# Kernel optimization log

Hardware: AMD Instinct MI355X
Metric: run time of the kernel (lower is better)

The kernel has to match this reference:

```python
import jax, jax.numpy as jnp
import numpy as np

B, L, HID = 128, 256, 768
HID2 = 2 * HID
CDIM, SDIM, NPROJ = 192, 128, 128
FDIM = CDIM + SDIM + 1
BIG = 1e9  # finite pad so sorted invalid tokens go last without inf/nan issues


def setup_inputs() -> dict:
    key = jax.random.key(0)
    ks = jax.random.split(key, 12)
    H = jax.random.normal(ks[0], (B, L, HID), dtype=jnp.float32)
    tt = jax.random.randint(ks[1], (B, L), 0, 2, dtype=jnp.int32)
    m = jnp.ones((B, L), dtype=jnp.int32)
    s = 1.0 / np.sqrt(HID2)
    Wc = jax.random.uniform(ks[2], (CDIM, HID2), minval=-s, maxval=s, dtype=jnp.float32)
    bc = jax.random.uniform(ks[3], (CDIM,), minval=-s, maxval=s, dtype=jnp.float32)
    Ws = jax.random.uniform(ks[4], (SDIM, HID2), minval=-s, maxval=s, dtype=jnp.float32)
    bs = jax.random.uniform(ks[5], (SDIM,), minval=-s, maxval=s, dtype=jnp.float32)
    gate = jnp.array([0.5], dtype=jnp.float32)
    ln_g = jnp.ones((FDIM,), dtype=jnp.float32)
    ln_b = jnp.zeros((FDIM,), dtype=jnp.float32)
    sc = 1.0 / np.sqrt(FDIM)
    Wcls = jax.random.uniform(ks[6], (2, FDIM), minval=-sc, maxval=sc, dtype=jnp.float32)
    bcls = jax.random.uniform(ks[7], (2,), minval=-sc, maxval=sc, dtype=jnp.float32)
    d = jax.random.normal(ks[8], (NPROJ, HID), dtype=jnp.float32)
    proj_dirs = d / jnp.linalg.norm(d, axis=1, keepdims=True)
    return {"H": H, "tt": tt, "m": m, "Wc": Wc, "bc": bc, "Ws": Ws, "bs": bs,
            "gate": gate, "ln_g": ln_g, "ln_b": ln_b, "Wcls": Wcls, "bcls": bcls,
            "proj_dirs": proj_dirs}


def _forward(H, tt, m, Wc, bc, Ws, bs, gate, ln_g, ln_b, Wcls, bcls, proj_dirs):
    mask0 = (tt == 0) & (m == 1)  # [B,L]
    mask1 = (tt == 1) & (m == 1)
    f0 = mask0.astype(H.dtype)
    f1 = mask1.astype(H.dtype)
    cls = H[:, 0]  # [B,HID]
    mean0 = jnp.einsum('blh,bl->bh', H, f0) / jnp.clip(f0.sum(1, keepdims=True), 1.0)
    mean1 = jnp.einsum('blh,bl->bh', H, f1) / jnp.clip(f1.sum(1, keepdims=True), 1.0)
    rep = jnp.concatenate([cls, mean0 - mean1], axis=1)  # [B,2*HID]
    C = rep @ Wc.T + bc
    S = rep @ Ws.T + bs
    g = jax.nn.sigmoid(gate)  # [1]
    fused = jnp.concatenate([C * (1.0 - g), S * g], axis=1)

    # max-sliced W1 between token-type-0 and token-type-1 token sets, batched.
    P = jnp.einsum('blh,ph->blp', H, proj_dirs)  # [B,L,NPROJ]
    x0 = jnp.sort(jnp.where(mask0[..., None], P, BIG), axis=1)  # valid tokens first
    x1 = jnp.sort(jnp.where(mask1[..., None], P, BIG), axis=1)
    n0 = mask0.sum(1)
    n1 = mask1.sum(1)
    mcnt = jnp.minimum(n0, n1)  # [B]
    rmask = (jnp.arange(L)[None, :] < mcnt[:, None])[..., None]  # [B,L,1]
    diff = jnp.where(rmask, x0, 0.0) - jnp.where(rmask, x1, 0.0)
    mean_abs = jnp.abs(diff).sum(1) / jnp.maximum(mcnt, 1)[:, None].astype(P.dtype)  # [B,NPROJ]
    d_ot = mean_abs.max(axis=1, keepdims=True)  # [B,1]

    feat = jnp.concatenate([fused, d_ot], axis=1)  # [B,FDIM]
    mu = feat.mean(-1, keepdims=True)
    var = feat.var(-1, keepdims=True)
    normed = (feat - mu) * jax.lax.rsqrt(var + 1e-5) * ln_g + ln_b
    return normed @ Wcls.T + bcls  # [B,2]


def reference(H, tt, m, Wc, bc, Ws, bs, gate, ln_g, ln_b, Wcls, bcls, proj_dirs):
    return _forward(H, tt, m, Wc, bc, Ws, bs, gate, ln_g, ln_b, Wcls, bcls, proj_dirs)
```

## Files before the change

kernel.cpp:

```cpp
#include <hip/hip_runtime.h>
#include <cmath>

#define B_   128
#define L_   256
#define HID_ 768
#define HID2_ 1536
#define CDIM_ 192
#define SDIM_ 128
#define NPROJ_ 128
#define FDIM_ 321

typedef __attribute__((ext_vector_type(8))) short bf16x8;
typedef __attribute__((ext_vector_type(4))) float f32x4;

__device__ inline unsigned short bf_hi_trunc(float x) {
    return (unsigned short)(__float_as_uint(x) >> 16);
}
__device__ inline float bf2f(unsigned short s) {
    return __uint_as_float(((unsigned int)s) << 16);
}
__device__ inline unsigned short f2bf_rne(float x) {
    unsigned int u = __float_as_uint(x);
    unsigned int r = (u + 0x7fff + ((u >> 16) & 1)) >> 16;
    return (unsigned short)r;
}

__global__ __launch_bounds__(192) void stats_part(
    const float* __restrict__ H, const int* __restrict__ tt,
    const int* __restrict__ mm, float* __restrict__ part)
{
    int b  = blockIdx.x >> 3;
    int pr = blockIdx.x & 7;
    int tid = threadIdx.x;

    __shared__ float sf0[32], sf1[32];
    if (tid < 32) {
        int l = pr * 32 + tid;
        int t = tt[b * L_ + l];
        int mv = mm[b * L_ + l];
        sf0[tid] = (t == 0 && mv == 1) ? 1.f : 0.f;
        sf1[tid] = (t == 1 && mv == 1) ? 1.f : 0.f;
    }
    __syncthreads();

    const float* Hb = H + ((size_t)(b * L_ + pr * 32)) * HID_;
    float4 a0 = make_float4(0.f, 0.f, 0.f, 0.f);
    float4 a1 = make_float4(0.f, 0.f, 0.f, 0.f);
    for (int l = 0; l < 32; ++l) {
        float4 x = *(const float4*)(Hb + (size_t)l * HID_ + tid * 4);
        float f0 = sf0[l], f1 = sf1[l];
        a0.x += x.x * f0; a0.y += x.y * f0; a0.z += x.z * f0; a0.w += x.w * f0;
        a1.x += x.x * f1; a1.y += x.y * f1; a1.z += x.z * f1; a1.w += x.w * f1;
    }
    float* dst = part + ((size_t)(b * 8 + pr)) * HID2_;
    *(float4*)(dst + tid * 4) = a0;
    *(float4*)(dst + HID_ + tid * 4) = a1;
}

__global__ __launch_bounds__(256) void stats_fin(
    const float* __restrict__ H, const int* __restrict__ tt,
    const int* __restrict__ mm, const float* __restrict__ part,
    float* __restrict__ rep)
{
    int b = blockIdx.x;
    int tid = threadIdx.x;
    int t = tt[b * L_ + tid];
    int mv = mm[b * L_ + tid];
    int n0 = __syncthreads_count(t == 0 && mv == 1);
    int n1 = __syncthreads_count(t == 1 && mv == 1);
    float r0 = 1.f / fmaxf((float)n0, 1.f);
    float r1 = 1.f / fmaxf((float)n1, 1.f);

    const float* pp = part + (size_t)b * 8 * HID2_;
    for (int h = tid; h < HID_; h += 256) {
        float a0 = 0.f, a1 = 0.f;
#pragma unroll
        for (int q = 0; q < 8; ++q) {
            a0 += pp[(size_t)q * HID2_ + h];
            a1 += pp[(size_t)q * HID2_ + HID_ + h];
        }
        rep[(size_t)b * HID2_ + h] = H[(size_t)b * L_ * HID_ + h];
        rep[(size_t)b * HID2_ + HID_ + h] = a0 * r0 - a1 * r1;
    }
}

__global__ __launch_bounds__(256) void head_kernel(
    const float* __restrict__ rep, const float* __restrict__ Wc,
    const float* __restrict__ bc, const float* __restrict__ Ws,
    const float* __restrict__ bs, const float* __restrict__ gate,
    float* __restrict__ fused)
{
    int w = blockIdx.x * 4 + (threadIdx.x >> 6);
    int lane = threadIdx.x & 63;
    int b = w / (CDIM_ + SDIM_);
    int o = w % (CDIM_ + SDIM_);
    bool isC = (o < CDIM_);
    const float4* wr = (const float4*)(isC ? (Wc + (size_t)o * HID2_)
                                           : (Ws + (size_t)(o - CDIM_) * HID2_));
    const float4* rp = (const float4*)(rep + (size_t)b * HID2_);
    float acc = 0.f;
#pragma unroll
    for (int u = 0; u < 6; ++u) {
        int k4 = lane + u * 64;
        float4 a = rp[k4];
        float4 ww = wr[k4];
        acc += a.x * ww.x + a.y * ww.y + a.z * ww.z + a.w * ww.w;
    }
    for (int off = 32; off; off >>= 1) acc += __shfl_xor(acc, off, 64);
    if (lane == 0) {
        float g = 1.0f / (1.0f + expf(-gate[0]));
        float bias = isC ? bc[o] : bs[o - CDIM_];
        float scale = isC ? (1.0f - g) : g;
        fused[(size_t)b * (CDIM_ + SDIM_) + o] = (acc + bias) * scale;
    }
}

__global__ __launch_bounds__(256) void conv_proj(
    const float* __restrict__ Pd, unsigned short* __restrict__ hi,
    unsigned short* __restrict__ lo)
{
    int i = blockIdx.x * 256 + threadIdx.x;
    float4 v = ((const float4*)Pd)[i];
    ushort4 h, l;
    h.x = bf_hi_trunc(v.x); l.x = f2bf_rne(v.x - bf2f(h.x));
    h.y = bf_hi_trunc(v.y); l.y = f2bf_rne(v.y - bf2f(h.y));
    h.z = bf_hi_trunc(v.z); l.z = f2bf_rne(v.z - bf2f(h.z));
    h.w = bf_hi_trunc(v.w); l.w = f2bf_rne(v.w - bf2f(h.w));
    ((ushort4*)hi)[i] = h;
    ((ushort4*)lo)[i] = l;
}

#define LDSROW 72
__global__ __launch_bounds__(256, 2) void gemm_mfma(
    const float* __restrict__ H, const unsigned short* __restrict__ Pjh,
    const unsigned short* __restrict__ Pjl, float* __restrict__ Pt)
{
    __shared__ unsigned short Hs[2][64 * LDSROW];

    int tid = threadIdx.x;
    int w = tid >> 6;
    int lane = tid & 63;
    int c = lane & 15;
    int q = lane >> 4;

    int b = blockIdx.x >> 2;
    int lbase = (blockIdx.x & 3) * 64;

    const float* Hbase = H + ((size_t)(b * L_ + lbase)) * HID_;

    int hrow0 = tid >> 3;
    int hc4   = tid & 7;

    const unsigned short* pjh0 = Pjh + (size_t)(w * 32 + c) * HID_ + q * 8;
    const unsigned short* pjh1 = Pjh + (size_t)(w * 32 + 16 + c) * HID_ + q * 8;
    const unsigned short* pjl0 = Pjl + (size_t)(w * 32 + c) * HID_ + q * 8;
    const unsigned short* pjl1 = Pjl + (size_t)(w * 32 + 16 + c) * HID_ + q * 8;

    f32x4 acc[2][4] = {};

    float4 hreg[2];
    uint4 cah[2], cal[2];
    uint4 nah[2], nal[2];

    hreg[0] = *(const float4*)(Hbase + (size_t)hrow0 * HID_ + hc4 * 4);
    hreg[1] = *(const float4*)(Hbase + (size_t)(hrow0 + 32) * HID_ + hc4 * 4);
    cah[0] = *(const uint4*)(pjh0);
    cah[1] = *(const uint4*)(pjh1);
    cal[0] = *(const uint4*)(pjl0);
    cal[1] = *(const uint4*)(pjl1);
#pragma unroll
    for (int u = 0; u < 2; ++u) {
        int row = hrow0 + u * 32;
        float4 v = hreg[u];
        ushort4 h, l;
        h.x = bf_hi_trunc(v.x); l.x = f2bf_rne(v.x - bf2f(h.x));
        h.y = bf_hi_trunc(v.y); l.y = f2bf_rne(v.y - bf2f(h.y));
        h.z = bf_hi_trunc(v.z); l.z = f2bf_rne(v.z - bf2f(h.z));
        h.w = bf_hi_trunc(v.w); l.w = f2bf_rne(v.w - bf2f(h.w));
        *(ushort4*)&Hs[0][row * LDSROW + hc4 * 4]      = h;
        *(ushort4*)&Hs[0][row * LDSROW + 32 + hc4 * 4] = l;
    }
    __syncthreads();

    for (int it = 0; it < 24; ++it) {
        int cur = it & 1;
        int nxt = cur ^ 1;

        if (it + 1 < 24) {
            int k0 = (it + 1) * 32;
            hreg[0] = *(const float4*)(Hbase + (size_t)hrow0 * HID_ + k0 + hc4 * 4);
            hreg[1] = *(const float4*)(Hbase + (size_t)(hrow0 + 32) * HID_ + k0 + hc4 * 4);
            nah[0] = *(const uint4*)(pjh0 + k0);
            nah[1] = *(const uint4*)(pjh1 + k0);
            nal[0] = *(const uint4*)(pjl0 + k0);
            nal[1] = *(const uint4*)(pjl1 + k0);
        }

        bf16x8 bh[4], bl[4];
#pragma unroll
        for (int lt = 0; lt < 4; ++lt) {
            int l = lt * 16 + c;
            bh[lt] = *(const bf16x8*)&Hs[cur][l * LDSROW + q * 8];
            bl[lt] = *(const bf16x8*)&Hs[cur][l * LDSROW + 32 + q * 8];
        }
        bf16x8 ah[2], al[2];
        ah[0] = *(bf16x8*)&cah[0]; ah[1] = *(bf16x8*)&cah[1];
        al[0] = *(bf16x8*)&cal[0]; al[1] = *(bf16x8*)&cal[1];

#pragma unroll
        for (int pt = 0; pt < 2; ++pt)
#pragma unroll
        for (int lt = 0; lt < 4; ++lt) {
            acc[pt][lt] = __builtin_amdgcn_mfma_f32_16x16x32_bf16(ah[pt], bh[lt], acc[pt][lt], 0, 0, 0);
            acc[pt][lt] = __builtin_amdgcn_mfma_f32_16x16x32_bf16(ah[pt], bl[lt], acc[pt][lt], 0, 0, 0);
            acc[pt][lt] = __builtin_amdgcn_mfma_f32_16x16x32_bf16(al[pt], bh[lt], acc[pt][lt], 0, 0, 0);
        }

        if (it + 1 < 24) {
#pragma unroll
            for (int u = 0; u < 2; ++u) {
                int row = hrow0 + u * 32;
                float4 v = hreg[u];
                ushort4 h, l;
                h.x = bf_hi_trunc(v.x); l.x = f2bf_rne(v.x - bf2f(h.x));
                h.y = bf_hi_trunc(v.y); l.y = f2bf_rne(v.y - bf2f(h.y));
                h.z = bf_hi_trunc(v.z); l.z = f2bf_rne(v.z - bf2f(h.z));
                h.w = bf_hi_trunc(v.w); l.w = f2bf_rne(v.w - bf2f(h.w));
                *(ushort4*)&Hs[nxt][row * LDSROW + hc4 * 4]      = h;
                *(ushort4*)&Hs[nxt][row * LDSROW + 32 + hc4 * 4] = l;
            }
            cah[0] = nah[0]; cah[1] = nah[1];
            cal[0] = nal[0]; cal[1] = nal[1];
        }
        __syncthreads();
    }

#pragma unroll
    for (int pt = 0; pt < 2; ++pt)
#pragma unroll
    for (int lt = 0; lt < 4; ++lt)
#pragma unroll
    for (int r = 0; r < 4; ++r) {
        int p = w * 32 + pt * 16 + q * 4 + r;
        int l = lbase + lt * 16 + c;
        Pt[((size_t)(b * NPROJ_ + p)) * L_ + l] = acc[pt][lt][r];
    }
}

__global__ __launch_bounds__(256) void ot_kernel(
    const float* __restrict__ Pt, const int* __restrict__ tt,
    const int* __restrict__ mm, float* __restrict__ dist)
{
    int w = blockIdx.x * 4 + (threadIdx.x >> 6);
    int lane = threadIdx.x & 63;
    int b = w >> 7;
    int p = w & (NPROJ_ - 1);

    float4 pv = *(const float4*)(Pt + ((size_t)(b * NPROJ_ + p)) * L_ + lane * 4);
    int4 t4 = *(const int4*)(tt + (size_t)b * L_ + lane * 4);
    int4 m4 = *(const int4*)(mm + (size_t)b * L_ + lane * 4);

    float pvals[4] = {pv.x, pv.y, pv.z, pv.w};
    int tv[4] = {t4.x, t4.y, t4.z, t4.w};
    int mv[4] = {m4.x, m4.y, m4.z, m4.w};

    unsigned key[4];
#pragma unroll
    for (int r = 0; r < 4; ++r) {
        unsigned u = __float_as_uint(pvals[r]);
        unsigned s = (u & 0x80000000u) ? ~u : (u | 0x80000000u);
        unsigned label = (mv[r] == 1) ? (unsigned)tv[r] : 2u;
        key[r] = (s & ~3u) | label;
    }

    {
        unsigned mn0 = min(key[0], key[1]), mx0 = max(key[0], key[1]);
        key[0] = mn0; key[1] = mx0;
        unsigned mn1 = min(key[2], key[3]), mx1 = max(key[2], key[3]);
        key[2] = mx1; key[3] = mn1;
    }
#pragma unroll
    for (int k = 4; k <= 256; k <<= 1) {
        bool up = (lane & (k >> 2)) == 0;
#pragma unroll
        for (int j = k >> 1; j >= 4; j >>= 1) {
            int lj = j >> 2;
#pragma unroll
            for (int r = 0; r < 4; ++r) {
                unsigned o = (unsigned)__shfl_xor((int)key[r], lj, 64);
                bool lower = (lane & lj) == 0;
                unsigned mn = min(key[r], o), mx = max(key[r], o);
                key[r] = (lower == up) ? mn : mx;
            }
        }
        {
            unsigned mn0 = min(key[0], key[2]), mx0 = max(key[0], key[2]);
            key[0] = up ? mn0 : mx0; key[2] = up ? mx0 : mn0;
            unsigned mn1 = min(key[1], key[3]), mx1 = max(key[1], key[3]);
            key[1] = up ? mn1 : mx1; key[3] = up ? mx1 : mn1;
        }
        {
            unsigned mn0 = min(key[0], key[1]), mx0 = max(key[0], key[1]);
            key[0] = up ? mn0 : mx0; key[1] = up ? mx0 : mn0;
            unsigned mn1 = min(key[2], key[3]), mx1 = max(key[2], key[3]);
            key[2] = up ? mn1 : mx1; key[3] = up ? mx1 : mn1;
        }
    }

    int lab[4];
    float tval[4];
    unsigned sincl[4];
    unsigned run = 0;
#pragma unroll
    for (int r = 0; r < 4; ++r) {
        lab[r] = (int)(key[r] & 3u);
        unsigned s = key[r] & ~3u;
        unsigned u = (s & 0x80000000u) ? (s ^ 0x80000000u) : ~s;
        tval[r] = __uint_as_float(u);
        unsigned unit = ((lab[r] == 0) ? 0x10000u : 0u) | ((lab[r] == 1) ? 1u : 0u);
        run += unit;
        sincl[r] = run;
    }
    unsigned inc = run;
#pragma unroll
    for (int d = 1; d < 64; d <<= 1) {
        unsigned t = (unsigned)__shfl_up((int)inc, d, 64);
        if (lane >= d) inc += t;
    }
    unsigned ex = inc - run;
    unsigned total = (unsigned)__shfl((int)inc, 63, 64);
    int n0 = (int)(total >> 16), n1 = (int)(total & 0xffffu);
    int m = (n0 < n1) ? n0 : n1;

    float ssum = 0.f;
#pragma unroll
    for (int r = 0; r < 4; ++r) {
        unsigned C = ex + sincl[r];
        int c0 = (int)(C >> 16), c1 = (int)(C & 0xffffu);
        int s0 = (lab[r] == 0), s1 = (lab[r] == 1);
        int wi = abs(min(c0, m) - min(c1, m));
        int wp = abs(min(c0 - s0, m) - min(c1 - s1, m));
        ssum += tval[r] * (float)(wp - wi);
    }
    for (int off = 32; off; off >>= 1) ssum += __shfl_xor(ssum, off, 64);
    if (lane == 0) dist[b * NPROJ_ + p] = ssum / (float)((m > 1) ? m : 1);
}

__global__ __launch_bounds__(64) void final_kernel(
    const float* __restrict__ fused, const float* __restrict__ dist,
    const float* __restrict__ ln_g, const float* __restrict__ ln_b,
    const float* __restrict__ Wcls, const float* __restrict__ bcls,
    float* __restrict__ out)
{
    int b = blockIdx.x;
    int lane = threadIdx.x;

    float mx = fmaxf(dist[b * NPROJ_ + lane], dist[b * NPROJ_ + 64 + lane]);
    for (int off = 32; off; off >>= 1) mx = fmaxf(mx, __shfl_xor(mx, off, 64));

    float fv[6];
    float sum = 0.f, sq = 0.f;
#pragma unroll
    for (int u = 0; u < 6; ++u) {
        int j = lane + u * 64;
        float x = 0.f;
        if (j < CDIM_ + SDIM_) x = fused[(size_t)b * (CDIM_ + SDIM_) + j];
        else if (j == CDIM_ + SDIM_) x = mx;
        fv[u] = x;
        if (j < FDIM_) { sum += x; sq += x * x; }
    }
    for (int off = 32; off; off >>= 1) {
        sum += __shfl_xor(sum, off, 64);
        sq  += __shfl_xor(sq,  off, 64);
    }
    float mu = sum / (float)FDIM_;
    float var = sq / (float)FDIM_ - mu * mu;
    float inv = rsqrtf(var + 1e-5f);

    float d0 = 0.f, d1 = 0.f;
#pragma unroll
    for (int u = 0; u < 6; ++u) {
        int j = lane + u * 64;
        if (j < FDIM_) {
            float nx = (fv[u] - mu) * inv * ln_g[j] + ln_b[j];
            d0 += nx * Wcls[j];
            d1 += nx * Wcls[FDIM_ + j];
        }
    }
    for (int off = 32; off; off >>= 1) {
        d0 += __shfl_xor(d0, off, 64);
        d1 += __shfl_xor(d1, off, 64);
    }
    if (lane == 0) {
        out[b * 2 + 0] = d0 + bcls[0];
        out[b * 2 + 1] = d1 + bcls[1];
    }
}

extern "C" void kernel_launch(void* const* d_in, const int* in_sizes, int n_in,
                              void* d_out, int out_size, void* d_ws, size_t ws_size,
                              hipStream_t stream)
{
    const float* H    = (const float*)d_in[0];
    const int*   tt   = (const int*)d_in[1];
    const int*   mm   = (const int*)d_in[2];
    const float* Wc   = (const float*)d_in[3];
    const float* bc   = (const float*)d_in[4];
    const float* Ws   = (const float*)d_in[5];
    const float* bs   = (const float*)d_in[6];
    const float* gate = (const float*)d_in[7];
    const float* ln_g = (const float*)d_in[8];
    const float* ln_b = (const float*)d_in[9];
    const float* Wcls = (const float*)d_in[10];
    const float* bcls = (const float*)d_in[11];
    const float* Pd   = (const float*)d_in[12];
    float* out = (float*)d_out;

    float* ws = (float*)d_ws;
    float* Pt    = ws;
    float* part  = Pt;
    float* rep   = Pt + (size_t)B_ * NPROJ_ * L_;
    float* fused = rep + (size_t)B_ * HID2_;
    float* dist  = fused + (size_t)B_ * (CDIM_ + SDIM_);
    unsigned short* Pjh = (unsigned short*)(dist + (size_t)B_ * NPROJ_);
    unsigned short* Pjl = Pjh + (size_t)NPROJ_ * HID_;

    conv_proj<<<NPROJ_ * HID_ / 4 / 256, 256, 0, stream>>>(Pd, Pjh, Pjl);
    stats_part<<<B_ * 8, 192, 0, stream>>>(H, tt, mm, part);
    stats_fin<<<B_, 256, 0, stream>>>(H, tt, mm, part, rep);
    head_kernel<<<B_ * (CDIM_ + SDIM_) / 4, 256, 0, stream>>>(rep, Wc, bc, Ws, bs, gate, fused);
    gemm_mfma<<<B_ * 4, 256, 0, stream>>>(H, Pjh, Pjl, Pt);
    ot_kernel<<<B_ * NPROJ_ / 4, 256, 0, stream>>>(Pt, tt, mm, dist);
    final_kernel<<<B_, 64, 0, stream>>>(fused, dist, ln_g, ln_b, Wcls, bcls, out);
}
```

Before: 248.6 us.

## Fuse projection conversion with stats, and stats finalize with classifier head

Merges the bf16 split of projection directions into the partial-stats kernel as extra blocks. It also merges the stats finalization and the C/S head matvec into one per-batch kernel that keeps the representation in shared memory. This removes two launches and the global rep buffer, and gives the partial sums their own workspace so they are no longer aliased with Pt. The cost is that the head now runs on only 128 blocks, each looping over 320 weight rows, which reduces parallelism.

```diff
diff --git a/kernel.cpp b/kernel.cpp
--- a/kernel.cpp
+++ b/kernel.cpp
@@ -25,13 +25,28 @@
     return (unsigned short)r;
 }
 
-__global__ __launch_bounds__(192) void stats_part(
+__global__ __launch_bounds__(192) void pre_kernel(
+    const float* __restrict__ Pd, unsigned short* __restrict__ Pjh,
+    unsigned short* __restrict__ Pjl,
     const float* __restrict__ H, const int* __restrict__ tt,
     const int* __restrict__ mm, float* __restrict__ part)
 {
-    int b  = blockIdx.x >> 3;
-    int pr = blockIdx.x & 7;
     int tid = threadIdx.x;
+    if (blockIdx.x < 128) {
+        int i = blockIdx.x * 192 + tid;
+        float4 v = ((const float4*)Pd)[i];
+        ushort4 h, l;
+        h.x = bf_hi_trunc(v.x); l.x = f2bf_rne(v.x - bf2f(h.x));
+        h.y = bf_hi_trunc(v.y); l.y = f2bf_rne(v.y - bf2f(h.y));
+        h.z = bf_hi_trunc(v.z); l.z = f2bf_rne(v.z - bf2f(h.z));
+        h.w = bf_hi_trunc(v.w); l.w = f2bf_rne(v.w - bf2f(h.w));
+        ((ushort4*)Pjh)[i] = h;
+        ((ushort4*)Pjl)[i] = l;
+        return;
+    }
+    int bid = blockIdx.x - 128;
+    int b  = bid >> 3;
+    int pr = bid & 7;
 
     __shared__ float sf0[32], sf1[32];
     if (tid < 32) {
@@ -55,79 +70,6 @@
     float* dst = part + ((size_t)(b * 8 + pr)) * HID2_;
     *(float4*)(dst + tid * 4) = a0;
     *(float4*)(dst + HID_ + tid * 4) = a1;
-}
-
-__global__ __launch_bounds__(256) void stats_fin(
-    const float* __restrict__ H, const int* __restrict__ tt,
-    const int* __restrict__ mm, const float* __restrict__ part,
-    float* __restrict__ rep)
-{
-    int b = blockIdx.x;
-    int tid = threadIdx.x;
-    int t = tt[b * L_ + tid];
-    int mv = mm[b * L_ + tid];
-    int n0 = __syncthreads_count(t == 0 && mv == 1);
-    int n1 = __syncthreads_count(t == 1 && mv == 1);
-    float r0 = 1.f / fmaxf((float)n0, 1.f);
-    float r1 = 1.f / fmaxf((float)n1, 1.f);
-
-    const float* pp = part + (size_t)b * 8 * HID2_;
-    for (int h = tid; h < HID_; h += 256) {
-        float a0 = 0.f, a1 = 0.f;
-#pragma unroll
-        for (int q = 0; q < 8; ++q) {
-            a0 += pp[(size_t)q * HID2_ + h];
-            a1 += pp[(size_t)q * HID2_ + HID_ + h];
-        }
-        rep[(size_t)b * HID2_ + h] = H[(size_t)b * L_ * HID_ + h];
-        rep[(size_t)b * HID2_ + HID_ + h] = a0 * r0 - a1 * r1;
-    }
-}
-
-__global__ __launch_bounds__(256) void head_kernel(
-    const float* __restrict__ rep, const float* __restrict__ Wc,
-    const float* __restrict__ bc, const float* __restrict__ Ws,
-    const float* __restrict__ bs, const float* __restrict__ gate,
-    float* __restrict__ fused)
-{
-    int w = blockIdx.x * 4 + (threadIdx.x >> 6);
-    int lane = threadIdx.x & 63;
-    int b = w / (CDIM_ + SDIM_);
-    int o = w % (CDIM_ + SDIM_);
-    bool isC = (o < CDIM_);
-    const float4* wr = (const float4*)(isC ? (Wc + (size_t)o * HID2_)
-                                           : (Ws + (size_t)(o - CDIM_) * HID2_));
-    const float4* rp = (const float4*)(rep + (size_t)b * HID2_);
-    float acc = 0.f;
-#pragma unroll
-    for (int u = 0; u < 6; ++u) {
-        int k4 = lane + u * 64;
-        float4 a = rp[k4];
-        float4 ww = wr[k4];
-        acc += a.x * ww.x + a.y * ww.y + a.z * ww.z + a.w * ww.w;
-    }
-    for (int off = 32; off; off >>= 1) acc += __shfl_xor(acc, off, 64);
-    if (lane == 0) {
-        float g = 1.0f / (1.0f + expf(-gate[0]));
-        float bias = isC ? bc[o] : bs[o - CDIM_];
-        float scale = isC ? (1.0f - g) : g;
-        fused[(size_t)b * (CDIM_ + SDIM_) + o] = (acc + bias) * scale;
-    }
-}
-
-__global__ __launch_bounds__(256) void conv_proj(
-    const float* __restrict__ Pd, unsigned short* __restrict__ hi,
-    unsigned short* __restrict__ lo)
-{
-    int i = blockIdx.x * 256 + threadIdx.x;
-    float4 v = ((const float4*)Pd)[i];
-    ushort4 h, l;
-    h.x = bf_hi_trunc(v.x); l.x = f2bf_rne(v.x - bf2f(h.x));
-    h.y = bf_hi_trunc(v.y); l.y = f2bf_rne(v.y - bf2f(h.y));
-    h.z = bf_hi_trunc(v.z); l.z = f2bf_rne(v.z - bf2f(h.z));
-    h.w = bf_hi_trunc(v.w); l.w = f2bf_rne(v.w - bf2f(h.w));
-    ((ushort4*)hi)[i] = h;
-    ((ushort4*)lo)[i] = l;
 }
 
 #define LDSROW 72
@@ -244,6 +186,63 @@
         int p = w * 32 + pt * 16 + q * 4 + r;
         int l = lbase + lt * 16 + c;
         Pt[((size_t)(b * NPROJ_ + p)) * L_ + l] = acc[pt][lt][r];
+    }
+}
+
+__global__ __launch_bounds__(256) void finhead_kernel(
+    const float* __restrict__ H, const int* __restrict__ tt,
+    const int* __restrict__ mm, const float* __restrict__ part,
+    const float* __restrict__ Wc, const float* __restrict__ bc,
+    const float* __restrict__ Ws, const float* __restrict__ bs,
+    const float* __restrict__ gate, float* __restrict__ fused)
+{
+    __shared__ float srep[HID2_];
+
+    int b = blockIdx.x;
+    int tid = threadIdx.x;
+    int t = tt[b * L_ + tid];
+    int mv = mm[b * L_ + tid];
+    int n0 = __syncthreads_count(t == 0 && mv == 1);
+    int n1 = __syncthreads_count(t == 1 && mv == 1);
+    float r0 = 1.f / fmaxf((float)n0, 1.f);
+    float r1 = 1.f / fmaxf((float)n1, 1.f);
+
+    const float* pp = part + (size_t)b * 8 * HID2_;
+    for (int h = tid; h < HID_; h += 256) {
+        float a0 = 0.f, a1 = 0.f;
+#pragma unroll
+        for (int q = 0; q < 8; ++q) {
+            a0 += pp[(size_t)q * HID2_ + h];
+            a1 += pp[(size_t)q * HID2_ + HID_ + h];
+        }
+        srep[h] = H[(size_t)b * L_ * HID_ + h];
+        srep[HID_ + h] = a0 * r0 - a1 * r1;
+    }
+    __syncthreads();
+
+    int w = tid >> 6;
+    int lane = tid & 63;
+    float g = 1.0f / (1.0f + expf(-gate[0]));
+
+    for (int i = 0; i < 80; ++i) {
+        int o = i * 4 + w;
+        bool isC = (o < CDIM_);
+        const float4* wr = (const float4*)(isC ? (Wc + (size_t)o * HID2_)
+                                               : (Ws + (size_t)(o - CDIM_) * HID2_));
+        float acc = 0.f;
+#pragma unroll
+        for (int u = 0; u < 6; ++u) {
+            int k4 = lane + u * 64;
+            float4 a = *(const float4*)&srep[k4 * 4];
+            float4 ww = wr[k4];
+            acc += a.x * ww.x + a.y * ww.y + a.z * ww.z + a.w * ww.w;
+        }
+        for (int off = 32; off; off >>= 1) acc += __shfl_xor(acc, off, 64);
+        if (lane == 0) {
+            float bias = isC ? bc[o] : bs[o - CDIM_];
+            float scale = isC ? (1.0f - g) : g;
+            fused[(size_t)b * (CDIM_ + SDIM_) + o] = (acc + bias) * scale;
+        }
     }
 }
 
@@ -418,18 +417,15 @@
 
     float* ws = (float*)d_ws;
     float* Pt    = ws;
-    float* part  = Pt;
-    float* rep   = Pt + (size_t)B_ * NPROJ_ * L_;
-    float* fused = rep + (size_t)B_ * HID2_;
+    float* part  = Pt + (size_t)B_ * NPROJ_ * L_;
+    float* fused = part + (size_t)B_ * 8 * HID2_;
     float* dist  = fused + (size_t)B_ * (CDIM_ + SDIM_);
     unsigned short* Pjh = (unsigned short*)(dist + (size_t)B_ * NPROJ_);
     unsigned short* Pjl = Pjh + (size_t)NPROJ_ * HID_;
 
-    conv_proj<<<NPROJ_ * HID_ / 4 / 256, 256, 0, stream>>>(Pd, Pjh, Pjl);
-    stats_part<<<B_ * 8, 192, 0, stream>>>(H, tt, mm, part);
-    stats_fin<<<B_, 256, 0, stream>>>(H, tt, mm, part, rep);
-    head_kernel<<<B_ * (CDIM_ + SDIM_) / 4, 256, 0, stream>>>(rep, Wc, bc, Ws, bs, gate, fused);
+    pre_kernel<<<128 + B_ * 8, 192, 0, stream>>>(Pd, Pjh, Pjl, H, tt, mm, part);
     gemm_mfma<<<B_ * 4, 256, 0, stream>>>(H, Pjh, Pjl, Pt);
+    finhead_kernel<<<B_, 256, 0, stream>>>(H, tt, mm, part, Wc, bc, Ws, bs, gate, fused);
     ot_kernel<<<B_ * NPROJ_ / 4, 256, 0, stream>>>(Pt, tt, mm, dist);
     final_kernel<<<B_, 64, 0, stream>>>(fused, dist, ln_g, ln_b, Wcls, bcls, out);
 }
```

After: 332.1 us. 1.34x slower.
